# Kernel tuning notes

Hardware: AMD Instinct MI355X
Metric: run time of the kernel (lower is better)

The kernel has to match this reference:

```python
import jax, jax.numpy as jnp
import numpy as np

H = 1024
E = 8
K = 2
N = 16384
LN_EPS = 1e-5


def _layernorm(h, g, b):
    m = jnp.mean(h, axis=-1, keepdims=True)
    v = jnp.mean(jnp.square(h - m), axis=-1, keepdims=True)
    return (h - m) * jax.lax.rsqrt(v + LN_EPS) * g + b


def setup_inputs() -> dict:
    key = jax.random.key(0)
    ks = jax.random.split(key, 8)
    s = 0.02
    return {
        "x": jax.random.normal(ks[0], (N, H), dtype=jnp.float32),
        "Wg": jax.random.normal(ks[1], (H, E), dtype=jnp.float32) * s,
        "bg": jnp.zeros((E,), dtype=jnp.float32),
        "W1": jax.random.normal(ks[2], (E, H, H), dtype=jnp.float32) * s,
        "b1": jnp.zeros((E, H), dtype=jnp.float32),
        "g1": jnp.ones((E, H), dtype=jnp.float32),
        "be1": jnp.zeros((E, H), dtype=jnp.float32),
        "W2": jax.random.normal(ks[3], (E, H, H), dtype=jnp.float32) * s,
        "b2": jnp.zeros((E, H), dtype=jnp.float32),
        "g2": jnp.ones((E, H), dtype=jnp.float32),
        "be2": jnp.zeros((E, H), dtype=jnp.float32),
    }


def reference(x, Wg, bg, W1, b1, g1, be1, W2, b2, g2, be2):
    # Gating: softmax over experts, top-k, renormalize
    gate_probs = jax.nn.softmax(x @ Wg + bg, axis=1)            # [N, E]
    tk_p, tk_i = jax.lax.top_k(gate_probs, K)                    # [N, K]
    tk_p = tk_p / (jnp.sum(tk_p, axis=1, keepdims=True) + 1e-9)
    # Dense per-expert combine weight (zero where expert not selected)
    w = jnp.sum(tk_p[:, :, None] * jax.nn.one_hot(tk_i, E, dtype=x.dtype), axis=1)  # [N, E]

    # ResidualBlock per expert, computed densely for all tokens (dropout = eval/no-op)
    h = jnp.einsum('nh,eho->eno', x, W1) + b1[:, None, :]        # [E, N, H]
    h = jax.nn.relu(_layernorm(h, g1[:, None, :], be1[:, None, :]))
    h = jnp.einsum('enh,eho->eno', h, W2) + b2[:, None, :]
    h = _layernorm(h, g2[:, None, :], be2[:, None, :])
    y = jax.nn.relu(x[None, :, :] + h)                           # [E, N, H]

    moe_out = jnp.einsum('ne,enh->nh', w, y)                     # [N, H]
    return moe_out, gate_probs
```

## Files before the change

kernel.cpp:

```cpp
#include <hip/hip_runtime.h>
#include <cstdint>
#include <cstddef>

constexpr int H_DIM = 1024;
constexpr int NE    = 8;
constexpr int NT    = 16384;
constexpr int NP    = NT * 2;

constexpr int BM = 128, BN = 128, BK = 32;
constexpr int NKT = H_DIM / BK;
constexpr int MAX_WG = (NP / BM + NE) * (H_DIM / BN);
constexpr int GEMM_GRID = 768;

typedef __attribute__((ext_vector_type(8)))  short          short8;
typedef __attribute__((ext_vector_type(8)))  unsigned short ushort8;
typedef __attribute__((ext_vector_type(4)))  float          f32x4;

__device__ __forceinline__ unsigned short f2bf(float f) {
  union { float f; uint32_t u; } c; c.f = f;
  uint32_t u = c.u;
  u = (u + 0x7fffu + ((u >> 16) & 1u)) >> 16;
  return (unsigned short)u;
}
__device__ __forceinline__ float bf2f(unsigned short h) {
  union { uint32_t u; float f; } c; c.u = ((uint32_t)h) << 16;
  return c.f;
}

__device__ __forceinline__ void gload16(const unsigned short* g, unsigned short* l) {
  __builtin_amdgcn_global_load_lds((const __attribute__((address_space(1))) void*)g,
                                   (__attribute__((address_space(3))) void*)l, 16, 0, 0);
}

__global__ __launch_bounds__(256) void prep_kernel(
    const float* __restrict__ X, const float* __restrict__ Wg,
    const float* __restrict__ bg, unsigned short* __restrict__ Xb,
    float* __restrict__ gate_out, int* __restrict__ tk_e, float* __restrict__ tk_w,
    const float* __restrict__ W1, const float* __restrict__ W2,
    unsigned short* __restrict__ T1, unsigned short* __restrict__ T2)
{
  __shared__ float tile[64][65];
  int b = blockIdx.x;
  if (b >= 4096) {
    int t = b - 4096;
    int zi = t >> 8;
    const float* W = (zi < 8) ? W1 : W2;
    unsigned short* T = (zi < 8) ? T1 : T2;
    int e  = zi & 7;
    int o0 = ((t >> 4) & 15) * 64;
    int h0 = (t & 15) * 64;
    int c  = threadIdx.x & 63;
    int r0 = (threadIdx.x >> 6) * 16;
    const float* src = W + ((size_t)e * H_DIM + h0) * H_DIM + o0;
#pragma unroll
    for (int i = 0; i < 16; ++i)
      tile[r0 + i][c] = src[(size_t)(r0 + i) * H_DIM + c];
    __syncthreads();
    unsigned short* dst = T + ((size_t)e * H_DIM + o0) * H_DIM + h0;
#pragma unroll
    for (int i = 0; i < 16; ++i)
      dst[(size_t)(r0 + i) * H_DIM + c] = f2bf(tile[c][r0 + i]);
    return;
  }

  int wid = threadIdx.x >> 6, lane = threadIdx.x & 63;
  int n = b * 4 + wid;
  const float* xr = X + (size_t)n * H_DIM;

  const float4* xp = (const float4*)(xr + lane * 16);
  float4 f0 = xp[0], f1 = xp[1], f2 = xp[2], f3 = xp[3];
  float v[16] = {f0.x,f0.y,f0.z,f0.w, f1.x,f1.y,f1.z,f1.w,
                 f2.x,f2.y,f2.z,f2.w, f3.x,f3.y,f3.z,f3.w};

  ushort8 u0, u1;
#pragma unroll
  for (int j = 0; j < 8; ++j) { u0[j] = f2bf(v[j]); u1[j] = f2bf(v[8 + j]); }
  ushort8* xb = (ushort8*)(Xb + (size_t)n * H_DIM + lane * 16);
  xb[0] = u0; xb[1] = u1;

  float acc[8];
#pragma unroll
  for (int e = 0; e < 8; ++e) acc[e] = 0.f;
#pragma unroll
  for (int j = 0; j < 16; ++j) {
    int h = lane * 16 + j;
    const float4* wg = (const float4*)(Wg + (size_t)h * 8);
    float4 a = wg[0], bb = wg[1];
    float xv = v[j];
    acc[0] += xv * a.x;  acc[1] += xv * a.y;  acc[2] += xv * a.z;  acc[3] += xv * a.w;
    acc[4] += xv * bb.x; acc[5] += xv * bb.y; acc[6] += xv * bb.z; acc[7] += xv * bb.w;
  }
#pragma unroll
  for (int m = 1; m < 64; m <<= 1) {
#pragma unroll
    for (int e = 0; e < 8; ++e) acc[e] += __shfl_xor(acc[e], m);
  }
#pragma unroll
  for (int e = 0; e < 8; ++e) acc[e] += bg[e];

  float mx = acc[0];
#pragma unroll
  for (int e = 1; e < 8; ++e) mx = fmaxf(mx, acc[e]);
  float g[8], s = 0.f;
#pragma unroll
  for (int e = 0; e < 8; ++e) { g[e] = __expf(acc[e] - mx); s += g[e]; }
  float inv = 1.f / s;
#pragma unroll
  for (int e = 0; e < 8; ++e) g[e] *= inv;

  int e0 = 0; float b0 = g[0];
#pragma unroll
  for (int e = 1; e < 8; ++e) if (g[e] > b0) { b0 = g[e]; e0 = e; }
  int e1 = -1; float b1v = -1.f;
#pragma unroll
  for (int e = 0; e < 8; ++e) if (e != e0 && g[e] > b1v) { b1v = g[e]; e1 = e; }
  float s2 = b0 + b1v + 1e-9f;

  if (lane == 0) {
    float4* gp = (float4*)(gate_out + (size_t)n * 8);
    gp[0] = make_float4(g[0], g[1], g[2], g[3]);
    gp[1] = make_float4(g[4], g[5], g[6], g[7]);
    tk_e[2 * n] = e0; tk_e[2 * n + 1] = e1;
    tk_w[2 * n] = b0 / s2; tk_w[2 * n + 1] = b1v / s2;
  }
}

__global__ __launch_bounds__(256) void hist_kernel(
    const int* __restrict__ tk_e, int* __restrict__ blockHist)
{
  __shared__ int h[8];
  if (threadIdx.x < 8) h[threadIdx.x] = 0;
  __syncthreads();
  int i0 = blockIdx.x * 512 + threadIdx.x;
  atomicAdd(&h[tk_e[i0]], 1);
  atomicAdd(&h[tk_e[i0 + 256]], 1);
  __syncthreads();
  if (threadIdx.x < 8) blockHist[blockIdx.x * 8 + threadIdx.x] = h[threadIdx.x];
}

__global__ void scan_worklist_kernel(const int* __restrict__ blockHist,
                                     int* __restrict__ blockBase,
                                     int* __restrict__ count, int* __restrict__ offs,
                                     int* __restrict__ wl, int* __restrict__ wlCount,
                                     int* __restrict__ gemmCtr)
{
  __shared__ int nmt[8], ebase[8], totalS;
  int e = threadIdx.x;
  if (e < 8) {
    int run = 0;
    for (int b = 0; b < 64; ++b) { blockBase[b * 8 + e] = run; run += blockHist[b * 8 + e]; }
    count[e] = run;
  }
  __syncthreads();
  if (threadIdx.x == 0) {
    int o = 0, wo = 0;
    for (int k = 0; k < 8; ++k) {
      offs[k] = o; o += count[k];
      nmt[k] = (count[k] + BM - 1) / BM;
      ebase[k] = wo; wo += nmt[k] * (H_DIM / BN);
    }
    totalS = wo; wlCount[0] = wo;
    gemmCtr[0] = 0; gemmCtr[1] = 0;
  }
  __syncthreads();
  if (e < 8) {
    int o = offs[e];
    for (int b = 0; b < 64; ++b) blockBase[b * 8 + e] += o;
  }
  int total = totalS;
  for (int i = threadIdx.x; i < total; i += blockDim.x) {
    int ee = 0;
    while (ee < 7 && i >= ebase[ee + 1]) ++ee;
    int loc = i - ebase[ee];
    int nt = loc / nmt[ee];
    int mt = loc - nt * nmt[ee];
    wl[i] = (ee << 20) | (nt << 16) | mt;
  }
}

__global__ __launch_bounds__(256) void place_kernel(
    const int* __restrict__ tk_e, const int* __restrict__ blockBase,
    int* __restrict__ pairTok, int* __restrict__ pairExp, int* __restrict__ slots)
{
  __shared__ int cur[8];
  if (threadIdx.x < 8) cur[threadIdx.x] = blockBase[blockIdx.x * 8 + threadIdx.x];
  __syncthreads();
#pragma unroll
  for (int j = 0; j < 2; ++j) {
    int i = blockIdx.x * 512 + j * 256 + threadIdx.x;
    int e = tk_e[i];
    int s = atomicAdd(&cur[e], 1);
    pairTok[s] = i >> 1; pairExp[s] = e; slots[i] = s;
  }
}

template<bool GATHER>
__global__ __launch_bounds__(256, 3) void gemmp_kernel(
    const unsigned short* __restrict__ Ab,
    const unsigned short* __restrict__ Bt,
    const float* __restrict__ bias,
    const int* __restrict__ pairTok,
    const int* __restrict__ count, const int* __restrict__ offs,
    const int* __restrict__ wl, const int* __restrict__ wlCount,
    int* __restrict__ ctr,
    unsigned short* __restrict__ Out)
{
  __shared__ unsigned short As[3 * 4096];
  __shared__ unsigned short Bs[3 * 4096];
  __shared__ int shIdx;

  const int total = wlCount[0];
  const int tid = threadIdx.x;
  const int wid = tid >> 6, l = tid & 63;
  const int wr = wid >> 1, wc = wid & 1;

  const int rsub = (l >> 2);
  const int kswz = ((l & 3) * 8) ^ (((l >> 5) & 1) << 4);
  const int loff = ((l & 15) * 64 + (l >> 4) * 16) ^ (((l >> 3) & 1) << 5);

  int e = 0, ntb = 0, mtb = 0, cnt = 0, base = 0;
  const unsigned short *apg0 = nullptr, *apg1 = nullptr, *bpg0 = nullptr, *bpg1 = nullptr;

  auto SETUP = [&](int widx) {
    int ent = wl[widx];
    e = ent >> 20; ntb = (ent >> 16) & 15; mtb = ent & 0xffff;
    cnt = count[e]; base = offs[e];
    int r0 = wid * 16 + rsub;
    int r1 = 64 + wid * 16 + rsub;
    int g0 = mtb * BM + r0; if (g0 >= cnt) g0 = cnt - 1;
    int g1 = mtb * BM + r1; if (g1 >= cnt) g1 = cnt - 1;
    size_t a0, a1;
    if (GATHER) { a0 = (size_t)pairTok[base + g0]; a1 = (size_t)pairTok[base + g1]; }
    else        { a0 = (size_t)(base + g0);        a1 = (size_t)(base + g1); }
    apg0 = Ab + a0 * H_DIM + kswz;
    apg1 = Ab + a1 * H_DIM + kswz;
    const unsigned short* bb = Bt + ((size_t)e * H_DIM + ntb * BN) * H_DIM + kswz;
    bpg0 = bb + (size_t)r0 * H_DIM;
    bpg1 = bb + (size_t)r1 * H_DIM;
  };

  auto STAGE = [&](int u, int slot) {
    unsigned short* ad = As + slot * 4096 + wid * 512;
    unsigned short* bd = Bs + slot * 4096 + wid * 512;
    gload16(apg0 + (size_t)u * BK, ad);
    gload16(apg1 + (size_t)u * BK, ad + 2048);
    gload16(bpg0 + (size_t)u * BK, bd);
    gload16(bpg1 + (size_t)u * BK, bd + 2048);
  };

  if (tid == 0) shIdx = atomicAdd(ctr, 1);
  __syncthreads();
  int idx = shIdx;
  if (idx >= total) return;

  SETUP(idx);
  STAGE(0, 0); STAGE(1, 1);

  while (true) {
    asm volatile("s_waitcnt vmcnt(4)" ::: "memory");
    __builtin_amdgcn_s_barrier();

    f32x4 acc[4][4] = {};

    int sl = 0, sstage = 2;
    for (int t = 0; t < NKT; ++t) {
      const char* aB = (const char*)As + sl * 8192 + wr * 4096 + loff;
      const char* bB = (const char*)Bs + sl * 8192 + wc * 4096 + loff;

      short8 af[4], bfr[4];
#pragma unroll
      for (int j = 0; j < 4; ++j) af[j] = *(const short8*)(aB + j * 1024);
#pragma unroll
      for (int r = 0; r < 4; ++r) bfr[r] = *(const short8*)(bB + r * 1024);

      if (t + 2 < NKT) STAGE(t + 2, sstage);

      __builtin_amdgcn_s_setprio(1);
#pragma unroll
      for (int j = 0; j < 4; ++j)
#pragma unroll
        for (int r = 0; r < 4; ++r)
          acc[j][r] = __builtin_amdgcn_mfma_f32_16x16x32_bf16(af[j], bfr[r], acc[j][r], 0, 0, 0);
      __builtin_amdgcn_s_setprio(0);

      if (t + 2 < NKT)       asm volatile("s_waitcnt vmcnt(4)" ::: "memory");
      else if (t + 2 == NKT) asm volatile("s_waitcnt vmcnt(0)" ::: "memory");
      __builtin_amdgcn_s_barrier();

      sl = (sl == 2) ? 0 : sl + 1;
      sstage = (sstage == 2) ? 0 : sstage + 1;
    }

    if (tid == 0) shIdx = atomicAdd(ctr, 1);
    __syncthreads();
    int nidx = shIdx;
    bool more = (nidx < total);

    int ce = e, cntb = ntb, cmtb = mtb, ccnt = cnt, cbase = base;
    if (more) { SETUP(nidx); STAGE(0, 0); STAGE(1, 1); }

    float bvv[4];
#pragma unroll
    for (int r = 0; r < 4; ++r)
      bvv[r] = bias[ce * H_DIM + cntb * BN + wc * 64 + r * 16 + (l & 15)];
#pragma unroll
    for (int j = 0; j < 4; ++j) {
      int grow0 = cmtb * BM + wr * 64 + j * 16 + (l >> 4) * 4;
#pragma unroll
      for (int r = 0; r < 4; ++r) {
        int gcol = cntb * BN + wc * 64 + r * 16 + (l & 15);
#pragma unroll
        for (int v = 0; v < 4; ++v) {
          int row = grow0 + v;
          if (row < ccnt)
            Out[(size_t)(cbase + row) * H_DIM + gcol] = f2bf(acc[j][r][v] + bvv[r]);
        }
      }
    }

    if (!more) return;
  }
}

__global__ __launch_bounds__(256) void ln_relu_kernel(
    unsigned short* __restrict__ buf, const float* __restrict__ gamma,
    const float* __restrict__ beta, const int* __restrict__ pairExp)
{
  int wid = threadIdx.x >> 6, lane = threadIdx.x & 63;
  int row = blockIdx.x * 4 + wid;
  int e = pairExp[row];
  unsigned short* r = buf + (size_t)row * H_DIM;
  ushort8 u0 = ((const ushort8*)r)[lane];
  ushort8 u1 = ((const ushort8*)r)[lane + 64];
  float v[16];
#pragma unroll
  for (int j = 0; j < 8; ++j) { v[j] = bf2f(u0[j]); v[8 + j] = bf2f(u1[j]); }
  float s = 0.f, ss = 0.f;
#pragma unroll
  for (int j = 0; j < 16; ++j) { s += v[j]; ss += v[j] * v[j]; }
#pragma unroll
  for (int m = 1; m < 64; m <<= 1) { s += __shfl_xor(s, m); ss += __shfl_xor(ss, m); }
  float mean = s * (1.f / 1024.f);
  float var  = ss * (1.f / 1024.f) - mean * mean;
  float rs   = rsqrtf(var + 1e-5f);

  int h0 = lane * 8, h1 = 512 + lane * 8;
  const float4* gp0 = (const float4*)(gamma + (size_t)e * H_DIM + h0);
  const float4* bp0 = (const float4*)(beta  + (size_t)e * H_DIM + h0);
  const float4* gp1 = (const float4*)(gamma + (size_t)e * H_DIM + h1);
  const float4* bp1 = (const float4*)(beta  + (size_t)e * H_DIM + h1);
  float4 ga = gp0[0], gb = gp0[1], gc = gp1[0], gd = gp1[1];
  float4 ba = bp0[0], bb = bp0[1], bc = bp1[0], bd = bp1[1];
  float gv[16] = {ga.x,ga.y,ga.z,ga.w, gb.x,gb.y,gb.z,gb.w,
                  gc.x,gc.y,gc.z,gc.w, gd.x,gd.y,gd.z,gd.w};
  float bv[16] = {ba.x,ba.y,ba.z,ba.w, bb.x,bb.y,bb.z,bb.w,
                  bc.x,bc.y,bc.z,bc.w, bd.x,bd.y,bd.z,bd.w};
#pragma unroll
  for (int j = 0; j < 8; ++j) {
    float t0 = fmaxf((v[j]     - mean) * rs * gv[j]     + bv[j],     0.f);
    float t1 = fmaxf((v[8 + j] - mean) * rs * gv[8 + j] + bv[8 + j], 0.f);
    u0[j] = f2bf(t0); u1[j] = f2bf(t1);
  }
  ((ushort8*)r)[lane] = u0; ((ushort8*)r)[lane + 64] = u1;
}

__global__ __launch_bounds__(256) void combine_kernel(
    const unsigned short* __restrict__ buf2, const float* __restrict__ X,
    const float* __restrict__ g2, const float* __restrict__ be2,
    const int* __restrict__ slots, const int* __restrict__ tk_e,
    const float* __restrict__ tk_w, float* __restrict__ out)
{
  int wid = threadIdx.x >> 6, lane = threadIdx.x & 63;
  int n = blockIdx.x * 4 + wid;
  int h0 = lane * 8, h1 = 512 + lane * 8;

  const float4* xp0 = (const float4*)(X + (size_t)n * H_DIM + h0);
  const float4* xp1 = (const float4*)(X + (size_t)n * H_DIM + h1);
  float4 xa = xp0[0], xb = xp0[1], xc = xp1[0], xd = xp1[1];
  float xv[16] = {xa.x,xa.y,xa.z,xa.w, xb.x,xb.y,xb.z,xb.w,
                  xc.x,xc.y,xc.z,xc.w, xd.x,xd.y,xd.z,xd.w};
  float o[16];
#pragma unroll
  for (int j = 0; j < 16; ++j) o[j] = 0.f;

#pragma unroll
  for (int k = 0; k < 2; ++k) {
    int slot = slots[2 * n + k];
    int e = tk_e[2 * n + k];
    float w = tk_w[2 * n + k];
    const unsigned short* r = buf2 + (size_t)slot * H_DIM;
    ushort8 u0 = ((const ushort8*)r)[lane];
    ushort8 u1 = ((const ushort8*)r)[lane + 64];
    float v[16];
#pragma unroll
    for (int j = 0; j < 8; ++j) { v[j] = bf2f(u0[j]); v[8 + j] = bf2f(u1[j]); }
    float s = 0.f, ss = 0.f;
#pragma unroll
    for (int j = 0; j < 16; ++j) { s += v[j]; ss += v[j] * v[j]; }
#pragma unroll
    for (int m = 1; m < 64; m <<= 1) { s += __shfl_xor(s, m); ss += __shfl_xor(ss, m); }
    float mean = s * (1.f / 1024.f);
    float var  = ss * (1.f / 1024.f) - mean * mean;
    float rs   = rsqrtf(var + 1e-5f);

    const float4* gp0 = (const float4*)(g2  + (size_t)e * H_DIM + h0);
    const float4* bp0 = (const float4*)(be2 + (size_t)e * H_DIM + h0);
    const float4* gp1 = (const float4*)(g2  + (size_t)e * H_DIM + h1);
    const float4* bp1 = (const float4*)(be2 + (size_t)e * H_DIM + h1);
    float4 ga = gp0[0], gb = gp0[1], gc = gp1[0], gd = gp1[1];
    float4 ba = bp0[0], bb = bp0[1], bc = bp1[0], bd = bp1[1];
    float gv[16] = {ga.x,ga.y,ga.z,ga.w, gb.x,gb.y,gb.z,gb.w,
                    gc.x,gc.y,gc.z,gc.w, gd.x,gd.y,gd.z,gd.w};
    float bvv[16] = {ba.x,ba.y,ba.z,ba.w, bb.x,bb.y,bb.z,bb.w,
                     bc.x,bc.y,bc.z,bc.w, bd.x,bd.y,bd.z,bd.w};
#pragma unroll
    for (int j = 0; j < 16; ++j) {
      float u = (v[j] - mean) * rs * gv[j] + bvv[j];
      float y = fmaxf(xv[j] + u, 0.f);
      o[j] += w * y;
    }
  }

  float4* op0 = (float4*)(out + (size_t)n * H_DIM + h0);
  float4* op1 = (float4*)(out + (size_t)n * H_DIM + h1);
  op0[0] = make_float4(o[0], o[1], o[2], o[3]);
  op0[1] = make_float4(o[4], o[5], o[6], o[7]);
  op1[0] = make_float4(o[8], o[9], o[10], o[11]);
  op1[1] = make_float4(o[12], o[13], o[14], o[15]);
}

extern "C" void kernel_launch(void* const* d_in, const int* in_sizes, int n_in,
                              void* d_out, int out_size, void* d_ws, size_t ws_size,
                              hipStream_t stream)
{
  const float* x   = (const float*)d_in[0];
  const float* Wg  = (const float*)d_in[1];
  const float* bg  = (const float*)d_in[2];
  const float* W1  = (const float*)d_in[3];
  const float* b1  = (const float*)d_in[4];
  const float* g1  = (const float*)d_in[5];
  const float* be1 = (const float*)d_in[6];
  const float* W2  = (const float*)d_in[7];
  const float* b2  = (const float*)d_in[8];
  const float* g2  = (const float*)d_in[9];
  const float* be2 = (const float*)d_in[10];
  float* out = (float*)d_out;
  float* gate_out = out + (size_t)NT * H_DIM;

  char* ws = (char*)d_ws;
  size_t off = 0;
  auto alloc = [&](size_t bytes) { char* p = ws + off; off += (bytes + 255) & ~(size_t)255; return p; };
  unsigned short* w1bt = (unsigned short*)alloc((size_t)NE * H_DIM * H_DIM * 2);
  unsigned short* w2bt = (unsigned short*)alloc((size_t)NE * H_DIM * H_DIM * 2);
  unsigned short* buf1 = (unsigned short*)alloc((size_t)NP * H_DIM * 2);
  unsigned short* buf2 = (unsigned short*)alloc((size_t)NP * H_DIM * 2);
  int*   tk_e      = (int*)alloc((size_t)NP * 4);
  float* tk_w      = (float*)alloc((size_t)NP * 4);
  int*   pairTok   = (int*)alloc((size_t)NP * 4);
  int*   pairExp   = (int*)alloc((size_t)NP * 4);
  int*   slots     = (int*)alloc((size_t)NP * 4);
  int*   blockHist = (int*)alloc(64 * 8 * 4);
  int*   blockBase = (int*)alloc(64 * 8 * 4);
  int*   count     = (int*)alloc(8 * 4);
  int*   offs      = (int*)alloc(8 * 4);
  int*   wl        = (int*)alloc(MAX_WG * 4);
  int*   wlCount   = (int*)alloc(4);
  int*   gemmCtr   = (int*)alloc(2 * 4);
  (void)in_sizes; (void)n_in; (void)out_size; (void)ws_size;

  unsigned short* Xb = buf2;

  prep_kernel<<<dim3(8192), 256, 0, stream>>>(
      x, Wg, bg, Xb, gate_out, tk_e, tk_w, W1, W2, w1bt, w2bt);
  hist_kernel<<<dim3(64), 256, 0, stream>>>(tk_e, blockHist);
  scan_worklist_kernel<<<dim3(1), 256, 0, stream>>>(
      blockHist, blockBase, count, offs, wl, wlCount, gemmCtr);
  place_kernel<<<dim3(64), 256, 0, stream>>>(tk_e, blockBase, pairTok, pairExp, slots);
  gemmp_kernel<true><<<dim3(GEMM_GRID), 256, 0, stream>>>(
      Xb, w1bt, b1, pairTok, count, offs, wl, wlCount, gemmCtr + 0, buf1);
  ln_relu_kernel<<<dim3(NP / 4), 256, 0, stream>>>(buf1, g1, be1, pairExp);
  gemmp_kernel<false><<<dim3(GEMM_GRID), 256, 0, stream>>>(
      buf1, w2bt, b2, pairTok, count, offs, wl, wlCount, gemmCtr + 1, buf2);
  combine_kernel<<<dim3(NT / 4), 256, 0, stream>>>(
      buf2, x, g2, be2, slots, tk_e, tk_w, out);
}
```

Before: 421.6 us.

## Replace persistent atomic-scheduled GEMM with one-tile-per-block, XCD-aware mapping and 4-stage pipeline

Drops the persistent work-stealing loop and its atomic counter. The grouped GEMM now launches one workgroup per worklist tile, remapping block IDs so that consecutive tiles land on the same XCD for L2 reuse. The LDS ring buffer grows from 3 to 4 stages with prefetch distance 3, which adds latency hiding but raises LDS use and may lower occupancy. Blocks past the tile count exit at once, and the epilogue no longer overlaps with the next tile's prefetch.

```diff
diff --git a/kernel.cpp b/kernel.cpp
--- a/kernel.cpp
+++ b/kernel.cpp
@@ -10,7 +10,6 @@
 constexpr int BM = 128, BN = 128, BK = 32;
 constexpr int NKT = H_DIM / BK;
 constexpr int MAX_WG = (NP / BM + NE) * (H_DIM / BN);
-constexpr int GEMM_GRID = 768;
 
 typedef __attribute__((ext_vector_type(8)))  short          short8;
 typedef __attribute__((ext_vector_type(8)))  unsigned short ushort8;
@@ -141,8 +140,7 @@
 __global__ void scan_worklist_kernel(const int* __restrict__ blockHist,
                                      int* __restrict__ blockBase,
                                      int* __restrict__ count, int* __restrict__ offs,
-                                     int* __restrict__ wl, int* __restrict__ wlCount,
-                                     int* __restrict__ gemmCtr)
+                                     int* __restrict__ wl, int* __restrict__ wlCount)
 {
   __shared__ int nmt[8], ebase[8], totalS;
   int e = threadIdx.x;
@@ -160,7 +158,6 @@
       ebase[k] = wo; wo += nmt[k] * (H_DIM / BN);
     }
     totalS = wo; wlCount[0] = wo;
-    gemmCtr[0] = 0; gemmCtr[1] = 0;
   }
   __syncthreads();
   if (e < 8) {
@@ -195,36 +192,37 @@
 }
 
 template<bool GATHER>
-__global__ __launch_bounds__(256, 3) void gemmp_kernel(
+__global__ __launch_bounds__(256, 3) void gemm4d_kernel(
     const unsigned short* __restrict__ Ab,
     const unsigned short* __restrict__ Bt,
     const float* __restrict__ bias,
     const int* __restrict__ pairTok,
     const int* __restrict__ count, const int* __restrict__ offs,
     const int* __restrict__ wl, const int* __restrict__ wlCount,
-    int* __restrict__ ctr,
     unsigned short* __restrict__ Out)
 {
-  __shared__ unsigned short As[3 * 4096];
-  __shared__ unsigned short Bs[3 * 4096];
-  __shared__ int shIdx;
+  __shared__ unsigned short As[4 * 4096];
+  __shared__ unsigned short Bs[4 * 4096];
 
   const int total = wlCount[0];
+  const int orig = blockIdx.x;
+  if (orig >= total) return;
+  const int qq = total >> 3, rr = total & 7;
+  const int xcd = orig & 7, sub = orig >> 3;
+  const int idx = (xcd < rr ? xcd * (qq + 1) : rr * (qq + 1) + (xcd - rr) * qq) + sub;
+  const int ent = wl[idx];
+  const int e = ent >> 20, ntb = (ent >> 16) & 15, mtb = ent & 0xffff;
+  const int cnt = count[e], base = offs[e];
+
   const int tid = threadIdx.x;
   const int wid = tid >> 6, l = tid & 63;
   const int wr = wid >> 1, wc = wid & 1;
 
   const int rsub = (l >> 2);
   const int kswz = ((l & 3) * 8) ^ (((l >> 5) & 1) << 4);
-  const int loff = ((l & 15) * 64 + (l >> 4) * 16) ^ (((l >> 3) & 1) << 5);
-
-  int e = 0, ntb = 0, mtb = 0, cnt = 0, base = 0;
-  const unsigned short *apg0 = nullptr, *apg1 = nullptr, *bpg0 = nullptr, *bpg1 = nullptr;
-
-  auto SETUP = [&](int widx) {
-    int ent = wl[widx];
-    e = ent >> 20; ntb = (ent >> 16) & 15; mtb = ent & 0xffff;
-    cnt = count[e]; base = offs[e];
+
+  const unsigned short *apg0, *apg1, *bpg0, *bpg1;
+  {
     int r0 = wid * 16 + rsub;
     int r1 = 64 + wid * 16 + rsub;
     int g0 = mtb * BM + r0; if (g0 >= cnt) g0 = cnt - 1;
@@ -237,7 +235,9 @@
     const unsigned short* bb = Bt + ((size_t)e * H_DIM + ntb * BN) * H_DIM + kswz;
     bpg0 = bb + (size_t)r0 * H_DIM;
     bpg1 = bb + (size_t)r1 * H_DIM;
-  };
+  }
+
+  const int loff = ((l & 15) * 64 + (l >> 4) * 16) ^ (((l >> 3) & 1) << 5);
 
   auto STAGE = [&](int u, int slot) {
     unsigned short* ad = As + slot * 4096 + wid * 512;
@@ -248,77 +248,57 @@
     gload16(bpg1 + (size_t)u * BK, bd + 2048);
   };
 
-  if (tid == 0) shIdx = atomicAdd(ctr, 1);
-  __syncthreads();
-  int idx = shIdx;
-  if (idx >= total) return;
-
-  SETUP(idx);
-  STAGE(0, 0); STAGE(1, 1);
-
-  while (true) {
-    asm volatile("s_waitcnt vmcnt(4)" ::: "memory");
+  STAGE(0, 0); STAGE(1, 1); STAGE(2, 2);
+  asm volatile("s_waitcnt vmcnt(8)" ::: "memory");
+  __builtin_amdgcn_s_barrier();
+
+  f32x4 acc[4][4] = {};
+
+#pragma unroll 4
+  for (int t = 0; t < NKT; ++t) {
+    const int sl = t & 3;
+    const char* aB = (const char*)As + sl * 8192 + wr * 4096 + loff;
+    const char* bB = (const char*)Bs + sl * 8192 + wc * 4096 + loff;
+
+    short8 af[4], bfr[4];
+#pragma unroll
+    for (int j = 0; j < 4; ++j) af[j] = *(const short8*)(aB + j * 1024);
+#pragma unroll
+    for (int r = 0; r < 4; ++r) bfr[r] = *(const short8*)(bB + r * 1024);
+
+    if (t + 3 < NKT) STAGE(t + 3, (t + 3) & 3);
+
+    __builtin_amdgcn_s_setprio(1);
+#pragma unroll
+    for (int j = 0; j < 4; ++j)
+#pragma unroll
+      for (int r = 0; r < 4; ++r)
+        acc[j][r] = __builtin_amdgcn_mfma_f32_16x16x32_bf16(af[j], bfr[r], acc[j][r], 0, 0, 0);
+    __builtin_amdgcn_s_setprio(0);
+
+    if (t + 3 < NKT)       asm volatile("s_waitcnt vmcnt(8)" ::: "memory");
+    else if (t + 3 == NKT) asm volatile("s_waitcnt vmcnt(4)" ::: "memory");
+    else if (t + 2 == NKT) asm volatile("s_waitcnt vmcnt(0)" ::: "memory");
     __builtin_amdgcn_s_barrier();
-
-    f32x4 acc[4][4] = {};
-
-    int sl = 0, sstage = 2;
-    for (int t = 0; t < NKT; ++t) {
-      const char* aB = (const char*)As + sl * 8192 + wr * 4096 + loff;
-      const char* bB = (const char*)Bs + sl * 8192 + wc * 4096 + loff;
-
-      short8 af[4], bfr[4];
-#pragma unroll
-      for (int j = 0; j < 4; ++j) af[j] = *(const short8*)(aB + j * 1024);
-#pragma unroll
-      for (int r = 0; r < 4; ++r) bfr[r] = *(const short8*)(bB + r * 1024);
-
-      if (t + 2 < NKT) STAGE(t + 2, sstage);
-
-      __builtin_amdgcn_s_setprio(1);
-#pragma unroll
-      for (int j = 0; j < 4; ++j)
-#pragma unroll
-        for (int r = 0; r < 4; ++r)
-          acc[j][r] = __builtin_amdgcn_mfma_f32_16x16x32_bf16(af[j], bfr[r], acc[j][r], 0, 0, 0);
-      __builtin_amdgcn_s_setprio(0);
-
-      if (t + 2 < NKT)       asm volatile("s_waitcnt vmcnt(4)" ::: "memory");
-      else if (t + 2 == NKT) asm volatile("s_waitcnt vmcnt(0)" ::: "memory");
-      __builtin_amdgcn_s_barrier();
-
-      sl = (sl == 2) ? 0 : sl + 1;
-      sstage = (sstage == 2) ? 0 : sstage + 1;
-    }
-
-    if (tid == 0) shIdx = atomicAdd(ctr, 1);
-    __syncthreads();
-    int nidx = shIdx;
-    bool more = (nidx < total);
-
-    int ce = e, cntb = ntb, cmtb = mtb, ccnt = cnt, cbase = base;
-    if (more) { SETUP(nidx); STAGE(0, 0); STAGE(1, 1); }
-
-    float bvv[4];
-#pragma unroll
-    for (int r = 0; r < 4; ++r)
-      bvv[r] = bias[ce * H_DIM + cntb * BN + wc * 64 + r * 16 + (l & 15)];
-#pragma unroll
-    for (int j = 0; j < 4; ++j) {
-      int grow0 = cmtb * BM + wr * 64 + j * 16 + (l >> 4) * 4;
-#pragma unroll
-      for (int r = 0; r < 4; ++r) {
-        int gcol = cntb * BN + wc * 64 + r * 16 + (l & 15);
-#pragma unroll
-        for (int v = 0; v < 4; ++v) {
-          int row = grow0 + v;
-          if (row < ccnt)
-            Out[(size_t)(cbase + row) * H_DIM + gcol] = f2bf(acc[j][r][v] + bvv[r]);
-        }
+  }
+
+  float bvv[4];
+#pragma unroll
+  for (int r = 0; r < 4; ++r)
+    bvv[r] = bias[e * H_DIM + ntb * BN + wc * 64 + r * 16 + (l & 15)];
+#pragma unroll
+  for (int j = 0; j < 4; ++j) {
+    int grow0 = mtb * BM + wr * 64 + j * 16 + (l >> 4) * 4;
+#pragma unroll
+    for (int r = 0; r < 4; ++r) {
+      int gcol = ntb * BN + wc * 64 + r * 16 + (l & 15);
+#pragma unroll
+      for (int v = 0; v < 4; ++v) {
+        int row = grow0 + v;
+        if (row < cnt)
+          Out[(size_t)(base + row) * H_DIM + gcol] = f2bf(acc[j][r][v] + bvv[r]);
       }
     }
-
-    if (!more) return;
   }
 }
 
@@ -465,7 +445,6 @@
   int*   offs      = (int*)alloc(8 * 4);
   int*   wl        = (int*)alloc(MAX_WG * 4);
   int*   wlCount   = (int*)alloc(4);
-  int*   gemmCtr   = (int*)alloc(2 * 4);
   (void)in_sizes; (void)n_in; (void)out_size; (void)ws_size;
 
   unsigned short* Xb = buf2;
@@ -474,13 +453,13 @@
       x, Wg, bg, Xb, gate_out, tk_e, tk_w, W1, W2, w1bt, w2bt);
   hist_kernel<<<dim3(64), 256, 0, stream>>>(tk_e, blockHist);
   scan_worklist_kernel<<<dim3(1), 256, 0, stream>>>(
-      blockHist, blockBase, count, offs, wl, wlCount, gemmCtr);
+      blockHist, blockBase, count, offs, wl, wlCount);
   place_kernel<<<dim3(64), 256, 0, stream>>>(tk_e, blockBase, pairTok, pairExp, slots);
-  gemmp_kernel<true><<<dim3(GEMM_GRID), 256, 0, stream>>>(
-      Xb, w1bt, b1, pairTok, count, offs, wl, wlCount, gemmCtr + 0, buf1);
+  gemm4d_kernel<true><<<dim3(MAX_WG), 256, 0, stream>>>(
+      Xb, w1bt, b1, pairTok, count, offs, wl, wlCount, buf1);
   ln_relu_kernel<<<dim3(NP / 4), 256, 0, stream>>>(buf1, g1, be1, pairExp);
-  gemmp_kernel<false><<<dim3(GEMM_GRID), 256, 0, stream>>>(
-      buf1, w2bt, b2, pairTok, count, offs, wl, wlCount, gemmCtr + 1, buf2);
+  gemm4d_kernel<false><<<dim3(MAX_WG), 256, 0, stream>>>(
+      buf1, w2bt, b2, pairTok, count, offs, wl, wlCount, buf2);
   combine_kernel<<<dim3(NT / 4), 256, 0, stream>>>(
       buf2, x, g2, be2, slots, tk_e, tk_w, out);
 }
```

Result: slower. 430.3 us (+2.1%).
